# Kernel optimization log

Hardware: AMD Instinct MI355X
Metric: run time of the kernel (lower is better)

Reference implementation:

```python
import jax, jax.numpy as jnp
import numpy as np

THRESHOLD = 1e-05
N = 4096

def setup_inputs() -> dict:
    key = jax.random.key(0)
    A = jax.random.normal(key, (N, N), dtype=jnp.float32)
    X = 0.5 * (A + A.T)  # symmetric so eigh is well-defined
    return {"X": X}

def reference(X):
    # ReEig: eigendecompose, clamp eigenvalues at threshold, reconstruct.
    eigval, U = jnp.linalg.eigh(X)          # eigval: [n], U: [n, n]
    eigval = jnp.maximum(eigval, jnp.asarray(THRESHOLD, X.dtype))
    # U @ diag(eigval) @ U.T, with the diag fused into a column scale
    return (U * eigval[None, :]) @ U.T
```

## Files before the change

kernel.cpp:

```cpp
#include <hip/hip_runtime.h>
#include <math.h>


#define N 4096
#define NN ((size_t)N * (size_t)N)
#define EPS 1e-5f
#define NITER 26

__global__ void fro_kernel(const float* __restrict__ X, float* __restrict__ scal) {
    __shared__ float red[4];
    int tid = threadIdx.x;
    size_t gid = (size_t)blockIdx.x * blockDim.x + tid;
    size_t stride = (size_t)gridDim.x * blockDim.x;
    const float4* X4 = (const float4*)X;
    size_t n4 = NN / 4;
    float s = 0.f;
    for (size_t i = gid; i < n4; i += stride) {
        float4 v = X4[i];
        s += v.x * v.x + v.y * v.y + v.z * v.z + v.w * v.w;
    }
    #pragma unroll
    for (int o = 32; o > 0; o >>= 1) s += __shfl_down(s, o, 64);
    int lane = tid & 63, wv = tid >> 6;
    if (lane == 0) red[wv] = s;
    __syncthreads();
    if (tid == 0) atomicAdd(&scal[0], red[0] + red[1] + red[2] + red[3]);
}

__global__ void schedule_kernel(float* __restrict__ scal) {
    if (threadIdx.x != 0 || blockIdx.x != 0) return;
    double c = sqrt((double)scal[0]);
    scal[1] = (float)c;
    double l = 1e-5 / c;
    const double KC = 2.598076211353316;
    for (int k = 0; k < NITER; ++k) {
        double s = 1.0 + l + l * l;
        double b = KC / (s * sqrt(s));
        double a = b * s;
        scal[2 + 2 * k] = (float)a;
        scal[3 + 2 * k] = (float)b;
        l = b * (s - 1.0);
        if (l > 1.0) l = 1.0;
    }
}

__global__ void init_kernel(const float* __restrict__ X, float* __restrict__ Y,
                            const float* __restrict__ scal) {
    float inv_c = 1.0f / scal[1];
    size_t gid = (size_t)blockIdx.x * blockDim.x + threadIdx.x;
    size_t stride = (size_t)gridDim.x * blockDim.x;
    const float4* X4 = (const float4*)X;
    float4* Y4 = (float4*)Y;
    size_t n4 = NN / 4;
    for (size_t i = gid; i < n4; i += stride) {
        float4 v = X4[i];
        size_t base = i * 4;
        int row = (int)(base >> 12);
        int col = (int)(base & 4095);
        int d = row - col;
        if (d >= 0 && d < 4) (&v.x)[d] -= EPS;
        v.x *= inv_c; v.y *= inv_c; v.z *= inv_c; v.w *= inv_c;
        Y4[i] = v;
    }
}

__launch_bounds__(256)
__global__ void gemm_kernel(const float* __restrict__ A, const float* __restrict__ B,
                            float* __restrict__ D, const float* __restrict__ E,
                            const float* __restrict__ scal, int k, int mode, int asub) {
    __shared__ float As[16][132];
    __shared__ float Bs[16][132];
    int tid = threadIdx.x;
    int lane = tid & 63;
    int wv = tid >> 6;
    int lx = lane & 7, ly = (lane >> 3) & 7;
    int wx = wv & 1, wy = wv >> 1;
    int bx = blockIdx.x, by = blockIdx.y;
    int row0 = by * 128 + wy * 64 + ly * 8;
    int col0 = bx * 128 + wx * 64 + lx * 8;

    float acc[8][8];
    #pragma unroll
    for (int i = 0; i < 8; ++i)
        #pragma unroll
        for (int j = 0; j < 8; ++j) acc[i][j] = 0.f;

    for (int kt = 0; kt < N; kt += 16) {
        #pragma unroll
        for (int h = 0; h < 2; ++h) {
            int q = tid + h * 256;
            int ra = q >> 2, ca = q & 3;
            int grow = by * 128 + ra;
            float4 va = *(const float4*)&A[(size_t)grow * N + kt + ca * 4];
            if (asub) {
                int d = grow - (kt + ca * 4);
                if (d >= 0 && d < 4) (&va.x)[d] -= EPS;
            }
            As[ca * 4 + 0][ra] = va.x;
            As[ca * 4 + 1][ra] = va.y;
            As[ca * 4 + 2][ra] = va.z;
            As[ca * 4 + 3][ra] = va.w;
            int rb = q >> 5, cb = q & 31;
            float4 vb = *(const float4*)&B[(size_t)(kt + rb) * N + bx * 128 + cb * 4];
            *(float4*)&Bs[rb][cb * 4] = vb;
        }
        __syncthreads();
        #pragma unroll
        for (int kk = 0; kk < 16; ++kk) {
            float4 a0 = *(const float4*)&As[kk][wy * 64 + ly * 8];
            float4 a1 = *(const float4*)&As[kk][wy * 64 + ly * 8 + 4];
            float4 b0 = *(const float4*)&Bs[kk][wx * 64 + lx * 8];
            float4 b1 = *(const float4*)&Bs[kk][wx * 64 + lx * 8 + 4];
            float av[8] = {a0.x, a0.y, a0.z, a0.w, a1.x, a1.y, a1.z, a1.w};
            float bv[8] = {b0.x, b0.y, b0.z, b0.w, b1.x, b1.y, b1.z, b1.w};
            #pragma unroll
            for (int i = 0; i < 8; ++i)
                #pragma unroll
                for (int j = 0; j < 8; ++j)
                    acc[i][j] = fmaf(av[i], bv[j], acc[i][j]);
        }
        __syncthreads();
    }

    float aa = 0.f, bb = 0.f;
    if (mode == 1) { aa = scal[2 + 2 * k]; bb = scal[3 + 2 * k]; }

    #pragma unroll
    for (int i = 0; i < 8; ++i) {
        int row = row0 + i;
        size_t off = (size_t)row * N + col0;
        float4 o0, o1;
        if (mode == 0) {
            o0 = make_float4(acc[i][0], acc[i][1], acc[i][2], acc[i][3]);
            o1 = make_float4(acc[i][4], acc[i][5], acc[i][6], acc[i][7]);
        } else if (mode == 1) {
            float4 e0 = *(const float4*)&E[off];
            float4 e1 = *(const float4*)&E[off + 4];
            o0 = make_float4(aa * e0.x - bb * acc[i][0], aa * e0.y - bb * acc[i][1],
                             aa * e0.z - bb * acc[i][2], aa * e0.w - bb * acc[i][3]);
            o1 = make_float4(aa * e1.x - bb * acc[i][4], aa * e1.y - bb * acc[i][5],
                             aa * e1.z - bb * acc[i][6], aa * e1.w - bb * acc[i][7]);
        } else {
            float4 e0 = *(const float4*)&E[off];
            float4 e1 = *(const float4*)&E[off + 4];
            float r[8];
            #pragma unroll
            for (int j = 0; j < 8; ++j) {
                float e = (j < 4) ? (&e0.x)[j] : (&e1.x)[j - 4];
                r[j] = 0.5f * e + 0.5f * acc[i][j];
                if (col0 + j == row) r[j] += 0.5f * EPS;
            }
            o0 = make_float4(r[0], r[1], r[2], r[3]);
            o1 = make_float4(r[4], r[5], r[6], r[7]);
        }
        *(float4*)&D[off] = o0;
        *(float4*)&D[off + 4] = o1;
    }
}

extern "C" void kernel_launch(void* const* d_in, const int* in_sizes, int n_in,
                              void* d_out, int out_size, void* d_ws, size_t ws_size,
                              hipStream_t stream) {
    const float* X = (const float*)d_in[0];
    float* out = (float*)d_out;
    float* ws0 = (float*)d_ws;
    float* ws1 = ws0 + NN;
    float* scal = ws1 + NN;

    hipMemsetAsync(scal, 0, 256 * sizeof(float), stream);
    fro_kernel<<<2048, 256, 0, stream>>>(X, scal);
    schedule_kernel<<<1, 64, 0, stream>>>(scal);
    init_kernel<<<2048, 256, 0, stream>>>(X, ws0, scal);

    float* buf[3] = {ws0, ws1, out};
    dim3 grid(N / 128, N / 128), blk(256);
    int p = 0;
    for (int k = 0; k < NITER; ++k) {
        float* Y  = buf[p];
        float* T  = buf[(p + 1) % 3];
        float* Yn = buf[(p + 2) % 3];
        gemm_kernel<<<grid, blk, 0, stream>>>(Y, Y, T, nullptr, scal, 0, 0, 0);
        gemm_kernel<<<grid, blk, 0, stream>>>(Y, T, Yn, Y, scal, k, 1, 0);
        p = (p + 2) % 3;
    }
    gemm_kernel<<<grid, blk, 0, stream>>>(X, buf[p], out, X, scal, 0, 2, 1);
}
```

Before: 94.61 ms.

## Add split-bf16 MFMA warm-start iterations before the fp32 polar iteration

Adds a pre-stage that stores the scaled iterate as hi/lo bf16 pairs and runs two polar/sign iterations with a 3-product split-bf16 MFMA GEMM. A sanitize pass then clamps the result, renormalises it and computes a new coefficient schedule, after which the original 26 fp32 SIMT iterations run from that warm start. The new path is only taken when the workspace is large enough. The fp32 iteration count is unchanged, so this adds four GEMMs and several elementwise passes without removing any fp32 work.

```diff
diff --git a/kernel.cpp b/kernel.cpp
--- a/kernel.cpp
+++ b/kernel.cpp
@@ -6,6 +6,21 @@
 #define NN ((size_t)N * (size_t)N)
 #define EPS 1e-5f
 #define NITER 26
+#define LDSROW 80
+#define LDSTILE (128 * LDSROW)
+
+typedef unsigned short u16;
+typedef unsigned int u32;
+typedef __attribute__((ext_vector_type(8))) short bf16x8;
+typedef __attribute__((ext_vector_type(4))) float f32x4;
+
+__device__ __forceinline__ float bf2f(u16 h) {
+    union { u32 u; float f; } c; c.u = ((u32)h) << 16; return c.f;
+}
+__device__ __forceinline__ u16 f2bf(float f) {
+    union { float f; u32 u; } c; c.f = f;
+    return (u16)((c.u + 0x7FFFu + ((c.u >> 16) & 1u)) >> 16);
+}
 
 __global__ void fro_kernel(const float* __restrict__ X, float* __restrict__ scal) {
     __shared__ float red[4];
@@ -41,6 +56,215 @@
         scal[3 + 2 * k] = (float)b;
         l = b * (s - 1.0);
         if (l > 1.0) l = 1.0;
+    }
+}
+
+__global__ void schedule2_kernel(float* __restrict__ scal) {
+    if (threadIdx.x != 0 || blockIdx.x != 0) return;
+    double c = sqrt((double)scal[60]);
+    float inv = (c > 1e-20) ? (float)(1.0 / c) : 0.f;
+    scal[61] = inv;
+    scal[62] = (float)c;
+    double l = (c > 1e-20) ? (1e-5 / c) : 1e-3;
+    const double KC = 2.598076211353316;
+    for (int k = 0; k < NITER; ++k) {
+        double s = 1.0 + l + l * l;
+        double b = KC / (s * sqrt(s));
+        double a = b * s;
+        scal[64 + 2 * k] = (float)a;
+        scal[65 + 2 * k] = (float)b;
+        l = b * (s - 1.0);
+        if (l > 1.0) l = 1.0;
+    }
+}
+
+__global__ void init_split_kernel(const float* __restrict__ X, u16* __restrict__ Hi,
+                                  u16* __restrict__ Lo, const float* __restrict__ scal) {
+    float inv_c = 1.0f / scal[1];
+    size_t gid = (size_t)blockIdx.x * blockDim.x + threadIdx.x;
+    size_t stride = (size_t)gridDim.x * blockDim.x;
+    const float4* X4 = (const float4*)X;
+    size_t n4 = NN / 4;
+    for (size_t i = gid; i < n4; i += stride) {
+        float4 v = X4[i];
+        size_t base = i * 4;
+        int row = (int)(base >> 12);
+        int col = (int)(base & 4095);
+        int d = row - col;
+        if (d >= 0 && d < 4) (&v.x)[d] -= EPS;
+        u16 h[4], l[4];
+        #pragma unroll
+        for (int j = 0; j < 4; ++j) {
+            float y = (&v.x)[j] * inv_c;
+            h[j] = f2bf(y);
+            l[j] = f2bf(y - bf2f(h[j]));
+        }
+        *(ushort4*)&Hi[base] = make_ushort4(h[0], h[1], h[2], h[3]);
+        *(ushort4*)&Lo[base] = make_ushort4(l[0], l[1], l[2], l[3]);
+    }
+}
+
+__device__ __forceinline__ float cleanv(u16 h, u16 l) {
+    float v = bf2f(h) + bf2f(l);
+    if (!isfinite(v)) v = 0.f;
+    return fminf(2.0f, fmaxf(-2.0f, v));
+}
+__global__ void san_pass1(const u16* __restrict__ Yh, const u16* __restrict__ Yl,
+                          float* __restrict__ scal) {
+    __shared__ float red[4];
+    int tid = threadIdx.x;
+    size_t gid = (size_t)blockIdx.x * blockDim.x + tid;
+    size_t stride = (size_t)gridDim.x * blockDim.x;
+    float s = 0.f;
+    size_t n4 = NN / 4;
+    for (size_t i = gid; i < n4; i += stride) {
+        size_t base = i * 4;
+        ushort4 h = *(const ushort4*)&Yh[base];
+        ushort4 l = *(const ushort4*)&Yl[base];
+        float v0 = cleanv(h.x, l.x), v1 = cleanv(h.y, l.y);
+        float v2 = cleanv(h.z, l.z), v3 = cleanv(h.w, l.w);
+        s += v0 * v0 + v1 * v1 + v2 * v2 + v3 * v3;
+    }
+    #pragma unroll
+    for (int o = 32; o > 0; o >>= 1) s += __shfl_down(s, o, 64);
+    int lane = tid & 63, wv = tid >> 6;
+    if (lane == 0) red[wv] = s;
+    __syncthreads();
+    if (tid == 0) atomicAdd(&scal[60], red[0] + red[1] + red[2] + red[3]);
+}
+__global__ void san_pass2(const u16* __restrict__ Yh, const u16* __restrict__ Yl,
+                          float* __restrict__ F, const float* __restrict__ scal) {
+    float sc = scal[61];
+    size_t gid = (size_t)blockIdx.x * blockDim.x + threadIdx.x;
+    size_t stride = (size_t)gridDim.x * blockDim.x;
+    size_t n4 = NN / 4;
+    for (size_t i = gid; i < n4; i += stride) {
+        size_t base = i * 4;
+        ushort4 h = *(const ushort4*)&Yh[base];
+        ushort4 l = *(const ushort4*)&Yl[base];
+        float4 o;
+        o.x = cleanv(h.x, l.x) * sc;
+        o.y = cleanv(h.y, l.y) * sc;
+        o.z = cleanv(h.z, l.z) * sc;
+        o.w = cleanv(h.w, l.w) * sc;
+        *(float4*)&F[base] = o;
+    }
+}
+
+__launch_bounds__(256)
+__global__ void gemm3_kernel(const u16* __restrict__ Ah, const u16* __restrict__ Al,
+                             const u16* __restrict__ Bh, const u16* __restrict__ Bl,
+                             const u16* __restrict__ Eh, const u16* __restrict__ El,
+                             const float* __restrict__ Xf, float* __restrict__ Dout,
+                             u16* __restrict__ Dh, u16* __restrict__ Dl,
+                             const float* __restrict__ scal, int kidx, int mode) {
+    __shared__ __align__(16) char smem[4 * LDSTILE];
+    int tid = threadIdx.x;
+    int lane = tid & 63;
+    int wv = tid >> 6;
+    int wr = wv >> 1, wc = wv & 1;
+    int bx = blockIdx.x, by = blockIdx.y;
+
+    int rs = tid >> 2;
+    int qs = tid & 3;
+    const u16* gptr[4][2];
+    char* lptr[4][2];
+    {
+        const u16* bases[4] = {Ah, Al, Bh, Bl};
+        #pragma unroll
+        for (int t = 0; t < 4; ++t) {
+            int row0 = (t < 2) ? by * 128 : bx * 128;
+            #pragma unroll
+            for (int h = 0; h < 2; ++h) {
+                int r = rs + h * 64;
+                gptr[t][h] = bases[t] + (size_t)(row0 + r) * N + qs * 8;
+                lptr[t][h] = smem + t * LDSTILE + r * LDSROW + qs * 16;
+            }
+        }
+    }
+
+    int q = lane >> 4;
+    u32 aoff[4], boff[4];
+    #pragma unroll
+    for (int m = 0; m < 4; ++m) {
+        int rf = wr * 64 + m * 16 + (lane & 15);
+        aoff[m] = (u32)(rf * LDSROW + q * 16);
+        int rg = wc * 64 + m * 16 + (lane & 15);
+        boff[m] = (u32)(rg * LDSROW + q * 16);
+    }
+
+    f32x4 acc[4][4];
+    #pragma unroll
+    for (int m = 0; m < 4; ++m)
+        #pragma unroll
+        for (int n = 0; n < 4; ++n) acc[m][n] = (f32x4){0.f, 0.f, 0.f, 0.f};
+
+    for (int kt = 0; kt < N; kt += 32) {
+        float4 stg[4][2];
+        #pragma unroll
+        for (int t = 0; t < 4; ++t)
+            #pragma unroll
+            for (int h = 0; h < 2; ++h) {
+                stg[t][h] = *(const float4*)gptr[t][h];
+                gptr[t][h] += 32;
+            }
+        __syncthreads();
+        #pragma unroll
+        for (int t = 0; t < 4; ++t)
+            #pragma unroll
+            for (int h = 0; h < 2; ++h)
+                *(float4*)lptr[t][h] = stg[t][h];
+        __syncthreads();
+
+        bf16x8 fah[4], fal[4], fbh[4], fbl[4];
+        #pragma unroll
+        for (int m = 0; m < 4; ++m) {
+            fah[m] = *(const bf16x8*)(smem + aoff[m]);
+            fal[m] = *(const bf16x8*)(smem + LDSTILE + aoff[m]);
+            fbh[m] = *(const bf16x8*)(smem + 2 * LDSTILE + boff[m]);
+            fbl[m] = *(const bf16x8*)(smem + 3 * LDSTILE + boff[m]);
+        }
+        #pragma unroll
+        for (int m = 0; m < 4; ++m)
+            #pragma unroll
+            for (int n = 0; n < 4; ++n) {
+                acc[m][n] = __builtin_amdgcn_mfma_f32_16x16x32_bf16(fah[m], fbh[n], acc[m][n], 0, 0, 0);
+                acc[m][n] = __builtin_amdgcn_mfma_f32_16x16x32_bf16(fah[m], fbl[n], acc[m][n], 0, 0, 0);
+                acc[m][n] = __builtin_amdgcn_mfma_f32_16x16x32_bf16(fal[m], fbh[n], acc[m][n], 0, 0, 0);
+            }
+    }
+
+    float ca = 0.f, cb = 0.f, hc = 0.f;
+    if (mode == 1) { ca = scal[2 + 2 * kidx]; cb = scal[3 + 2 * kidx]; }
+    if (mode == 2) { hc = 0.5f * scal[1]; }
+
+    #pragma unroll
+    for (int m = 0; m < 4; ++m) {
+        #pragma unroll
+        for (int n = 0; n < 4; ++n) {
+            #pragma unroll
+            for (int r = 0; r < 4; ++r) {
+                int grow = by * 128 + wr * 64 + m * 16 + (lane >> 4) * 4 + r;
+                int gcol = bx * 128 + wc * 64 + n * 16 + (lane & 15);
+                size_t idx = (size_t)grow * N + gcol;
+                float v = acc[m][n][r];
+                if (mode == 0) {
+                    u16 h = f2bf(v);
+                    Dh[idx] = h;
+                    Dl[idx] = f2bf(v - bf2f(h));
+                } else if (mode == 1) {
+                    float e = bf2f(Eh[idx]) + bf2f(El[idx]);
+                    float o = ca * e - cb * v;
+                    u16 h = f2bf(o);
+                    Dh[idx] = h;
+                    Dl[idx] = f2bf(o - bf2f(h));
+                } else {
+                    float o = 0.5f * Xf[idx] + hc * v;
+                    if (grow == gcol) o += 0.5f * EPS;
+                    Dout[idx] = o;
+                }
+            }
+        }
     }
 }
 
@@ -88,19 +312,19 @@
     for (int kt = 0; kt < N; kt += 16) {
         #pragma unroll
         for (int h = 0; h < 2; ++h) {
-            int q = tid + h * 256;
-            int ra = q >> 2, ca = q & 3;
+            int qq = tid + h * 256;
+            int ra = qq >> 2, caa = qq & 3;
             int grow = by * 128 + ra;
-            float4 va = *(const float4*)&A[(size_t)grow * N + kt + ca * 4];
+            float4 va = *(const float4*)&A[(size_t)grow * N + kt + caa * 4];
             if (asub) {
-                int d = grow - (kt + ca * 4);
+                int d = grow - (kt + caa * 4);
                 if (d >= 0 && d < 4) (&va.x)[d] -= EPS;
             }
-            As[ca * 4 + 0][ra] = va.x;
-            As[ca * 4 + 1][ra] = va.y;
-            As[ca * 4 + 2][ra] = va.z;
-            As[ca * 4 + 3][ra] = va.w;
-            int rb = q >> 5, cb = q & 31;
+            As[caa * 4 + 0][ra] = va.x;
+            As[caa * 4 + 1][ra] = va.y;
+            As[caa * 4 + 2][ra] = va.z;
+            As[caa * 4 + 3][ra] = va.w;
+            int rb = qq >> 5, cb = qq & 31;
             float4 vb = *(const float4*)&B[(size_t)(kt + rb) * N + bx * 128 + cb * 4];
             *(float4*)&Bs[rb][cb * 4] = vb;
         }
@@ -163,25 +387,68 @@
                               hipStream_t stream) {
     const float* X = (const float*)d_in[0];
     float* out = (float*)d_out;
-    float* ws0 = (float*)d_ws;
-    float* ws1 = ws0 + NN;
-    float* scal = ws1 + NN;
-
-    hipMemsetAsync(scal, 0, 256 * sizeof(float), stream);
-    fro_kernel<<<2048, 256, 0, stream>>>(X, scal);
-    schedule_kernel<<<1, 64, 0, stream>>>(scal);
-    init_kernel<<<2048, 256, 0, stream>>>(X, ws0, scal);
-
-    float* buf[3] = {ws0, ws1, out};
     dim3 grid(N / 128, N / 128), blk(256);
-    int p = 0;
-    for (int k = 0; k < NITER; ++k) {
-        float* Y  = buf[p];
-        float* T  = buf[(p + 1) % 3];
-        float* Yn = buf[(p + 2) % 3];
-        gemm_kernel<<<grid, blk, 0, stream>>>(Y, Y, T, nullptr, scal, 0, 0, 0);
-        gemm_kernel<<<grid, blk, 0, stream>>>(Y, T, Yn, Y, scal, k, 1, 0);
-        p = (p + 2) % 3;
-    }
-    gemm_kernel<<<grid, blk, 0, stream>>>(X, buf[p], out, X, scal, 0, 2, 1);
-}
+
+    size_t need_split = 1024 + 12 * NN;
+    if (ws_size >= need_split) {
+        float* scal = (float*)d_ws;
+        u16* b16 = (u16*)((char*)d_ws + 1024);
+        u16* Y0h = b16;
+        u16* Y0l = b16 + NN;
+        u16* Ph[3] = {b16 + 2 * NN, b16 + 4 * NN, (u16*)d_out};
+        u16* Pl[3] = {b16 + 3 * NN, b16 + 5 * NN, (u16*)d_out + NN};
+        float* f0 = (float*)b16;
+        float* f1 = (float*)(b16 + 2 * NN);
+
+        hipMemsetAsync(scal, 0, 256 * sizeof(float), stream);
+        fro_kernel<<<2048, 256, 0, stream>>>(X, scal);
+        schedule_kernel<<<1, 64, 0, stream>>>(scal);
+        init_split_kernel<<<2048, 256, 0, stream>>>(X, Y0h, Y0l, scal);
+
+        gemm3_kernel<<<grid, blk, 0, stream>>>(Y0h, Y0l, Y0h, Y0l, Y0h, Y0l, X, out,
+                                               Ph[0], Pl[0], scal, 0, 0);
+        gemm3_kernel<<<grid, blk, 0, stream>>>(Y0h, Y0l, Ph[0], Pl[0], Y0h, Y0l, X, out,
+                                               Ph[1], Pl[1], scal, 0, 1);
+        gemm3_kernel<<<grid, blk, 0, stream>>>(Ph[1], Pl[1], Ph[1], Pl[1], Ph[1], Pl[1],
+                                               X, out, Ph[2], Pl[2], scal, 0, 0);
+        gemm3_kernel<<<grid, blk, 0, stream>>>(Ph[1], Pl[1], Ph[2], Pl[2], Ph[1], Pl[1],
+                                               X, out, Ph[0], Pl[0], scal, 1, 1);
+
+        san_pass1<<<2048, 256, 0, stream>>>(Ph[0], Pl[0], scal);
+        schedule2_kernel<<<1, 64, 0, stream>>>(scal);
+        san_pass2<<<2048, 256, 0, stream>>>(Ph[0], Pl[0], f0, scal);
+
+        float* buf[3] = {f0, f1, out};
+        int q = 0;
+        for (int k = 0; k < NITER; ++k) {
+            float* Y  = buf[q];
+            float* T  = buf[(q + 1) % 3];
+            float* Yn = buf[(q + 2) % 3];
+            gemm_kernel<<<grid, blk, 0, stream>>>(Y, Y, T, nullptr, scal + 62, 0, 0, 0);
+            gemm_kernel<<<grid, blk, 0, stream>>>(Y, T, Yn, Y, scal + 62, k, 1, 0);
+            q = (q + 2) % 3;
+        }
+        gemm_kernel<<<grid, blk, 0, stream>>>(X, buf[q], out, X, scal, 0, 2, 1);
+    } else {
+        float* ws0 = (float*)d_ws;
+        float* ws1 = ws0 + NN;
+        float* scal = ws1 + NN;
+
+        hipMemsetAsync(scal, 0, 256 * sizeof(float), stream);
+        fro_kernel<<<2048, 256, 0, stream>>>(X, scal);
+        schedule_kernel<<<1, 64, 0, stream>>>(scal);
+        init_kernel<<<2048, 256, 0, stream>>>(X, ws0, scal);
+
+        float* buf[3] = {ws0, ws1, out};
+        int p = 0;
+        for (int k = 0; k < NITER; ++k) {
+            float* Y  = buf[p];
+            float* T  = buf[(p + 1) % 3];
+            float* Yn = buf[(p + 2) % 3];
+            gemm_kernel<<<grid, blk, 0, stream>>>(Y, Y, T, nullptr, scal, 0, 0, 0);
+            gemm_kernel<<<grid, blk, 0, stream>>>(Y, T, Yn, Y, scal, k, 1, 0);
+            p = (p + 2) % 3;
+        }
+        gemm_kernel<<<grid, blk, 0, stream>>>(X, buf[p], out, X, scal, 0, 2, 1);
+    }
+}
```

New measurement: 94.49 ms. Within noise of the previous version (-0.1%).
